# Kernel tuning notes

Measured on AMD Instinct MI355X. Metric: run time of the kernel, lower is better.

## Reference

```python
import jax, jax.numpy as jnp
import numpy as np

N_NODES = 100000
N_EDGES = 1600000
F_IN = 64
F_OUT = 64


def setup_inputs() -> dict:
    key = jax.random.key(0)
    ks = jax.random.split(key, 7)
    x_real = jax.random.normal(ks[0], (N_NODES, F_IN), dtype=jnp.float32)
    x_imag = jax.random.normal(ks[1], (N_NODES, F_IN), dtype=jnp.float32)
    weight = jax.random.normal(ks[2], (2, F_IN, F_OUT), dtype=jnp.float32) * (1.0 / np.sqrt(F_IN))
    bias = jax.random.normal(ks[3], (F_OUT,), dtype=jnp.float32) * 0.01
    norm_real = jax.random.normal(ks[4], (N_EDGES,), dtype=jnp.float32) * 0.1
    norm_imag = jax.random.normal(ks[5], (N_EDGES,), dtype=jnp.float32) * 0.1
    edge_index = jax.random.randint(ks[6], (2, N_EDGES), 0, N_NODES, dtype=jnp.int64 if jax.config.jax_enable_x64 else jnp.int32)
    return {
        "x_real": x_real,
        "x_imag": x_imag,
        "weight": weight,
        "bias": bias,
        "norm_real": norm_real,
        "norm_imag": norm_imag,
        "edge_index": edge_index,
    }


def reference(x_real, x_imag, weight, bias, norm_real, norm_imag, edge_index):
    # SigMaNetConv with i_complex=False: the K=0 term uses i_real=I, i_imag=0,
    # so real_real = x_real @ W0, imag_real = x_imag @ W0, cross terms vanish.
    n = x_real.shape[0]
    src = edge_index[0]  # aggregation target (flow: target_to_source semantics)
    dst = edge_index[1]  # neighbor being gathered (x_j)

    def prop(x, norm):
        # sparse Laplacian matvec: out[src] += norm * x[dst]  -> [N, F]
        return jax.ops.segment_sum(norm[:, None] * x[dst], src, num_segments=n)

    W0, W1 = weight[0], weight[1]
    out_real_real = x_real @ W0 + prop(x_real, norm_real) @ W1
    out_imag_imag = prop(x_imag, norm_imag) @ W1
    out_imag_real = x_imag @ W0 + prop(x_imag, norm_real) @ W1
    out_real_imag = prop(x_real, norm_imag) @ W1

    out_real = out_real_real - out_imag_imag + bias
    out_imag = out_imag_real + out_real_imag + bias
    return out_real, out_imag
```

## Files before the change

kernel.cpp:

```cpp
#include <hip/hip_runtime.h>

#define F 64
typedef unsigned int u32;
typedef unsigned long long u64;
typedef short bf16x8 __attribute__((ext_vector_type(8)));
typedef float f32x4 __attribute__((ext_vector_type(4)));

#define SCAN_BLOCK 1024
#define SCAN_ITEMS 4
#define NPART 8
#define EGRP 16
#define SLICE_MAX 12544
#define SPLITB 512
#define SITEMS 8

__device__ __forceinline__ u32 pack_bf16x2(float lo, float hi) {
    u32 a = __float_as_uint(lo);
    u32 b = __float_as_uint(hi);
    a = (a + 0x7fffu + ((a >> 16) & 1u)) >> 16;
    b = (b + 0x7fffu + ((b >> 16) & 1u)) >> 16;
    return a | (b << 16);
}
__device__ __forceinline__ float unpack_lo(u32 p) { return __uint_as_float(p << 16); }
__device__ __forceinline__ float unpack_hi(u32 p) { return __uint_as_float(p & 0xffff0000u); }

__global__ __launch_bounds__(256) void k_coarse(
    const int* __restrict__ src, int* __restrict__ bcnt,
    const float* __restrict__ weight, unsigned short* __restrict__ Btp,
    int n_edges, int slice, int chunk)
{
    const int t = threadIdx.x;
    if (blockIdx.x == SPLITB) {
        for (int i = t; i < 128 * 64; i += 256) {
            const int f2 = i >> 6;
            const int k  = i & 63;
            const float wv = weight[(f2 >= 64 ? F * F : 0) + k * F + (f2 & 63)];
            Btp[f2 * 64 + (((k >> 3) ^ (f2 & 7)) << 3) + (k & 7)] =
                (unsigned short)(pack_bf16x2(wv, 0.f) & 0xffffu);
        }
        return;
    }
    __shared__ int c[NPART];
    if (t < NPART) c[t] = 0;
    __syncthreads();
    const int cbeg = blockIdx.x * chunk;
    const int cend = min(cbeg + chunk, n_edges);
    for (int e = cbeg + t; e < cend; e += 256)
        atomicAdd(&c[(u32)src[e] / (u32)slice], 1);
    __syncthreads();
    if (t < NPART) bcnt[blockIdx.x * NPART + t] = c[t];
}

__global__ __launch_bounds__(SPLITB) void k_base2(
    const int* __restrict__ bcnt, int* __restrict__ bbase, int* __restrict__ pbase)
{
    __shared__ int wsum[SPLITB / 64];
    __shared__ int total[NPART];
    __shared__ int pb[NPART + 1];
    const int t = threadIdx.x;
    const int lane = t & 63, wid = t >> 6;

    for (int p = 0; p < NPART; ++p) {
        const int v = bcnt[t * NPART + p];
        int incl = v;
#pragma unroll
        for (int d = 1; d < 64; d <<= 1) {
            int x = __shfl_up(incl, d);
            if (lane >= d) incl += x;
        }
        if (lane == 63) wsum[wid] = incl;
        __syncthreads();
        if (wid == 0) {
            int s = (lane < SPLITB / 64) ? wsum[lane] : 0;
#pragma unroll
            for (int d = 1; d < SPLITB / 64; d <<= 1) {
                int x = __shfl_up(s, d);
                if (lane >= d) s += x;
            }
            if (lane < SPLITB / 64) wsum[lane] = s;
        }
        __syncthreads();
        const int excl = (incl - v) + (wid ? wsum[wid - 1] : 0);
        bbase[t * NPART + p] = excl;
        if (t == SPLITB - 1) total[p] = excl + v;
        __syncthreads();
    }
    if (t == 0) {
        int run = 0;
        for (int p = 0; p < NPART; ++p) { pb[p] = run; run += total[p]; }
        pb[NPART] = run;
        for (int p = 0; p <= NPART; ++p) pbase[p] = pb[p];
    }
    __syncthreads();
    for (int p = 0; p < NPART; ++p)
        bbase[t * NPART + p] += pb[p];
}

__global__ __launch_bounds__(256) void k_split(
    const int* __restrict__ ei, const float* __restrict__ nr, const float* __restrict__ ni,
    const int* __restrict__ bbase, u32* __restrict__ ssrc, u64* __restrict__ smrec,
    int n_edges, int slice, int chunk)
{
    __shared__ int cnt[NPART];
    __shared__ int gb[NPART];
    __shared__ int lcur[NPART];
    const int t = threadIdx.x;
    if (t < NPART) lcur[t] = bbase[blockIdx.x * NPART + t];
    const int cbeg = blockIdx.x * chunk;
    const int cend = min(cbeg + chunk, n_edges);

    for (int base = cbeg; base < cend; base += 256 * SITEMS) {
        if (t < NPART) cnt[t] = 0;
        __syncthreads();
        int p[SITEMS], lpos[SITEMS];
        u32 s[SITEMS]; u64 mrec[SITEMS];
#pragma unroll
        for (int j = 0; j < SITEMS; ++j) {
            const int e = base + t + 256 * j;
            if (e < cend) {
                s[j] = (u32)ei[e];
                const u32 d = (u32)ei[n_edges + e];
                const u32 nn = pack_bf16x2(nr[e], ni[e]);
                mrec[j] = (u64)d | ((u64)nn << 32);
                p[j] = (int)(s[j] / (u32)slice);
                lpos[j] = atomicAdd(&cnt[p[j]], 1);
            } else p[j] = -1;
        }
        __syncthreads();
        if (t < NPART) { gb[t] = lcur[t]; lcur[t] += cnt[t]; }
        __syncthreads();
#pragma unroll
        for (int j = 0; j < SITEMS; ++j) {
            if (p[j] >= 0) {
                const int gi = gb[p[j]] + lpos[j];
                ssrc[gi]  = s[j];
                smrec[gi] = mrec[j];
            }
        }
        __syncthreads();
    }
}

__global__ __launch_bounds__(1024) void k_hist8(
    const u32* __restrict__ ssrc, const int* __restrict__ pbase,
    int* __restrict__ priv, int n_nodes, int slice)
{
    __shared__ int h[SLICE_MAX];
    const int p = blockIdx.x & (NPART - 1);
    const int g = blockIdx.x >> 3;
    const int t = threadIdx.x;

    const int lo = p * slice;
    const int hi = min(lo + slice, n_nodes);
    const int sl = hi - lo;
    if (sl <= 0) return;

    for (int i = t; i < sl; i += 1024) h[i] = 0;
    __syncthreads();

    const int pb = pbase[p], pe = pbase[p + 1];
    const long long len = pe - pb;
    const int beg = pb + (int)(len * g / EGRP);
    const int end = pb + (int)(len * (g + 1) / EGRP);
    for (int e = beg + t; e < end; e += 1024)
        atomicAdd(&h[(int)ssrc[e] - lo], 1);
    __syncthreads();

    int* __restrict__ dst = priv + (size_t)g * n_nodes + lo;
    for (int i = t; i < sl; i += 1024) dst[i] = h[i];
}

__global__ __launch_bounds__(1024) void k_scan1(
    const int* __restrict__ priv, int* __restrict__ pre,
    int* __restrict__ partials, int n, int n_nodes)
{
    __shared__ int wsum[16];
    const int t = threadIdx.x;
    const int lane = t & 63, wid = t >> 6;
    const int base = blockIdx.x * (SCAN_BLOCK * SCAN_ITEMS) + t * SCAN_ITEMS;

    int v[SCAN_ITEMS];
    int local = 0;
#pragma unroll
    for (int j = 0; j < SCAN_ITEMS; ++j) {
        const int idx = base + j;
        int c = 0;
        if (idx < n) {
            for (int g = 0; g < EGRP; ++g) c += priv[(size_t)g * n_nodes + idx];
        }
        v[j] = local;
        local += c;
    }
    int incl = local;
#pragma unroll
    for (int d = 1; d < 64; d <<= 1) {
        int x = __shfl_up(incl, d);
        if (lane >= d) incl += x;
    }
    if (lane == 63) wsum[wid] = incl;
    __syncthreads();
    if (wid == 0) {
        int s = (lane < 16) ? wsum[lane] : 0;
#pragma unroll
        for (int d = 1; d < 16; d <<= 1) {
            int x = __shfl_up(s, d);
            if (lane >= d) s += x;
        }
        if (lane < 16) wsum[lane] = s;
    }
    __syncthreads();
    const int texcl = (incl - local) + (wid ? wsum[wid - 1] : 0);
#pragma unroll
    for (int j = 0; j < SCAN_ITEMS; ++j) {
        const int idx = base + j;
        if (idx < n) pre[idx] = texcl + v[j];
    }
    if (t == SCAN_BLOCK - 1) partials[blockIdx.x] = texcl + local;
}

__global__ __launch_bounds__(1024) void k_scan2(
    int* __restrict__ pre, const int* __restrict__ partials,
    int* __restrict__ po, int n, int n_nodes, int n_edges)
{
    __shared__ int s_off;
    const int t = threadIdx.x;
    if (t < 64) {
        int val = (t < blockIdx.x) ? partials[t] : 0;
#pragma unroll
        for (int d = 32; d > 0; d >>= 1) val += __shfl_down(val, d);
        if (t == 0) s_off = val;
    }
    __syncthreads();
    const int boff = s_off;
    const int base = blockIdx.x * (SCAN_BLOCK * SCAN_ITEMS) + t * SCAN_ITEMS;
#pragma unroll
    for (int j = 0; j < SCAN_ITEMS; ++j) {
        const int idx = base + j;
        if (idx < n) {
            const int o = boff + pre[idx];
            pre[idx] = o;
            int running = o;
            for (int g = 0; g < EGRP; ++g) {
                const size_t ix = (size_t)g * n_nodes + idx;
                const int c = po[ix];
                po[ix] = running;
                running += c;
            }
        }
    }
    if (blockIdx.x == 0 && t == 0) pre[n] = n_edges;
}

__global__ __launch_bounds__(1024) void k_place3(
    const u32* __restrict__ ssrc, const u64* __restrict__ smrec,
    const int* __restrict__ pbase, const int* __restrict__ off2,
    u64* __restrict__ meta2, int n_nodes, int slice)
{
    __shared__ int cur[SLICE_MAX];
    const int p = blockIdx.x & (NPART - 1);
    const int g = blockIdx.x >> 3;
    const int t = threadIdx.x;

    const int lo = p * slice;
    const int hi = min(lo + slice, n_nodes);
    const int sl = hi - lo;
    if (sl <= 0) return;

    const int* __restrict__ o2 = off2 + (size_t)g * n_nodes + lo;
    for (int i = t; i < sl; i += 1024) cur[i] = o2[i];
    __syncthreads();

    const int pb = pbase[p], pe = pbase[p + 1];
    const long long len = pe - pb;
    const int beg = pb + (int)(len * g / EGRP);
    const int end = pb + (int)(len * (g + 1) / EGRP);
    for (int e = beg + t; e < end; e += 1024) {
        const int s = (int)ssrc[e];
        const int pos = atomicAdd(&cur[s - lo], 1);
        meta2[pos] = smrec[e];
    }
}

__global__ __launch_bounds__(256, 4) void k_gemm(
    const float* __restrict__ x_real, const float* __restrict__ x_imag,
    const unsigned short* __restrict__ Btp, const float* __restrict__ bias,
    u32* __restrict__ x1p, u32* __restrict__ initp, int n_nodes)
{
    __shared__ unsigned short lds[2 * 128 * 64];
    unsigned short* __restrict__ A  = lds;
    unsigned short* __restrict__ Bt = lds + 128 * 64;

    const int t = threadIdx.x;
    const int base = blockIdx.x * 64;

#pragma unroll
    for (int c = 0; c < 8; ++c) {
        const int fq  = t + 256 * c;
        const int arr = fq >> 10;
        const int rem = fq & 1023;
        const int ln  = rem >> 4;
        const int c4  = rem & 15;
        const int g   = base + ln;
        const float* __restrict__ s = arr ? x_imag : x_real;
        float4 v = make_float4(0.f, 0.f, 0.f, 0.f);
        if (g < n_nodes) v = *(const float4*)(s + (size_t)g * F + c4 * 4);
        const int row  = 2 * ln + arr;
        const int kg   = c4 >> 1;
        const int half = c4 & 1;
        u32* dst = (u32*)&A[row * 64 + ((kg ^ (row & 7)) << 3) + (half << 2)];
        dst[0] = pack_bf16x2(v.x, v.y);
        dst[1] = pack_bf16x2(v.z, v.w);
    }

#pragma unroll
    for (int i = 0; i < 4; ++i) {
        const int idx = t + 256 * i;
        ((uint4*)Bt)[idx] = ((const uint4*)Btp)[idx];
    }
    __syncthreads();

    const int l   = t & 63;
    const int w   = t >> 6;
    const int l15 = l & 15;
    const int lg  = l >> 4;

    f32x4 acc[2][8];
#pragma unroll
    for (int tr = 0; tr < 2; ++tr)
#pragma unroll
        for (int tc = 0; tc < 8; ++tc)
            acc[tr][tc] = (f32x4){0.f, 0.f, 0.f, 0.f};

#pragma unroll
    for (int ks = 0; ks < 2; ++ks) {
        bf16x8 af[2];
#pragma unroll
        for (int tr = 0; tr < 2; ++tr) {
            const int row = w * 32 + tr * 16 + l15;
            const int kg  = ks * 4 + lg;
            af[tr] = *(const bf16x8*)&A[row * 64 + ((kg ^ (row & 7)) << 3)];
        }
#pragma unroll
        for (int tc = 0; tc < 8; ++tc) {
            const int f2 = tc * 16 + l15;
            const int kg = ks * 4 + lg;
            const bf16x8 bfr = *(const bf16x8*)&Bt[f2 * 64 + ((kg ^ (f2 & 7)) << 3)];
#pragma unroll
            for (int tr = 0; tr < 2; ++tr)
                acc[tr][tc] = __builtin_amdgcn_mfma_f32_16x16x32_bf16(
                    af[tr], bfr, acc[tr][tc], 0, 0, 0);
        }
    }

#pragma unroll
    for (int tc = 0; tc < 8; ++tc) {
        const int f2 = tc * 16 + l15;
        const float bv = (f2 < F) ? bias[f2] : 0.f;
#pragma unroll
        for (int tr = 0; tr < 2; ++tr) {
            const int row0 = w * 32 + tr * 16 + lg * 4;
            const int g0 = base + (row0 >> 1);
            const int g1 = g0 + 1;
            const f32x4 a = acc[tr][tc];
            if (f2 < F) {
                if (g0 < n_nodes) initp[(size_t)g0 * F + f2] = pack_bf16x2(a[0] + bv, a[1] + bv);
                if (g1 < n_nodes) initp[(size_t)g1 * F + f2] = pack_bf16x2(a[2] + bv, a[3] + bv);
            } else {
                const int f = f2 - F;
                if (g0 < n_nodes) x1p[(size_t)g0 * F + f] = pack_bf16x2(a[0], a[1]);
                if (g1 < n_nodes) x1p[(size_t)g1 * F + f] = pack_bf16x2(a[2], a[3]);
            }
        }
    }
}

#define APPLY2(m, p, aR, aI)                                  \
    do {                                                      \
        const u32 nnv = (u32)((m) >> 32);                     \
        const float cr = unpack_lo(nnv);                      \
        const float ci = unpack_hi(nnv);                      \
        const float xr = unpack_lo(p);                        \
        const float xi = unpack_hi(p);                        \
        aR = fmaf(cr, xr, fmaf(-ci, xi, aR));                 \
        aI = fmaf(cr, xi, fmaf(ci, xr, aI));                  \
    } while (0)

__global__ __launch_bounds__(256) void k_gather(
    const u32* __restrict__ x1p, const u32* __restrict__ initp,
    const int* __restrict__ offsets, const u64* __restrict__ meta2,
    float* __restrict__ out_real, float* __restrict__ out_imag,
    int n_nodes, int slice)
{
    const int part = blockIdx.x & (NPART - 1);
    const int lane = threadIdx.x & 63;
    const int wip = ((blockIdx.x >> 3) << 2) + (threadIdx.x >> 6);
    const int wpp = (gridDim.x >> 3) << 2;

    const int lo = part * slice;
    const int hi = min(lo + slice, n_nodes);
    if (hi <= lo) return;
    const int chunk = (hi - lo + wpp - 1) / wpp;
    const int nbeg = lo + wip * chunk;
    const int nend = min(nbeg + chunk, hi);

    for (int n = nbeg; n < nend; ++n) {
        const int nu = __builtin_amdgcn_readfirstlane(n);
        const int beg = __builtin_amdgcn_readfirstlane(offsets[nu]);
        const int end = __builtin_amdgcn_readfirstlane(offsets[nu + 1]);

        float aR0 = 0.f, aI0 = 0.f, aR1 = 0.f, aI1 = 0.f;
        float aR2 = 0.f, aI2 = 0.f, aR3 = 0.f, aI3 = 0.f;

        int e = beg;
        for (; e + 8 <= end; e += 8) {
            const u64 m0 = __builtin_nontemporal_load(meta2 + e + 0);
            const u64 m1 = __builtin_nontemporal_load(meta2 + e + 1);
            const u64 m2 = __builtin_nontemporal_load(meta2 + e + 2);
            const u64 m3 = __builtin_nontemporal_load(meta2 + e + 3);
            const u64 m4 = __builtin_nontemporal_load(meta2 + e + 4);
            const u64 m5 = __builtin_nontemporal_load(meta2 + e + 5);
            const u64 m6 = __builtin_nontemporal_load(meta2 + e + 6);
            const u64 m7 = __builtin_nontemporal_load(meta2 + e + 7);
            const u32 p0 = x1p[(size_t)(u32)m0 * F + lane];
            const u32 p1 = x1p[(size_t)(u32)m1 * F + lane];
            const u32 p2 = x1p[(size_t)(u32)m2 * F + lane];
            const u32 p3 = x1p[(size_t)(u32)m3 * F + lane];
            const u32 p4 = x1p[(size_t)(u32)m4 * F + lane];
            const u32 p5 = x1p[(size_t)(u32)m5 * F + lane];
            const u32 p6 = x1p[(size_t)(u32)m6 * F + lane];
            const u32 p7 = x1p[(size_t)(u32)m7 * F + lane];
            APPLY2(m0, p0, aR0, aI0);
            APPLY2(m1, p1, aR1, aI1);
            APPLY2(m2, p2, aR2, aI2);
            APPLY2(m3, p3, aR3, aI3);
            APPLY2(m4, p4, aR0, aI0);
            APPLY2(m5, p5, aR1, aI1);
            APPLY2(m6, p6, aR2, aI2);
            APPLY2(m7, p7, aR3, aI3);
        }
        for (; e + 4 <= end; e += 4) {
            const u64 m0 = __builtin_nontemporal_load(meta2 + e + 0);
            const u64 m1 = __builtin_nontemporal_load(meta2 + e + 1);
            const u64 m2 = __builtin_nontemporal_load(meta2 + e + 2);
            const u64 m3 = __builtin_nontemporal_load(meta2 + e + 3);
            const u32 p0 = x1p[(size_t)(u32)m0 * F + lane];
            const u32 p1 = x1p[(size_t)(u32)m1 * F + lane];
            const u32 p2 = x1p[(size_t)(u32)m2 * F + lane];
            const u32 p3 = x1p[(size_t)(u32)m3 * F + lane];
            APPLY2(m0, p0, aR0, aI0);
            APPLY2(m1, p1, aR1, aI1);
            APPLY2(m2, p2, aR2, aI2);
            APPLY2(m3, p3, aR3, aI3);
        }
        for (; e < end; ++e) {
            const u64 m = __builtin_nontemporal_load(meta2 + e);
            const u32 p = x1p[(size_t)(u32)m * F + lane];
            APPLY2(m, p, aR0, aI0);
        }

        const size_t b = (size_t)nu * F + lane;
        const u32 iw = __builtin_nontemporal_load(initp + b);
        const float oR = unpack_lo(iw) + ((aR0 + aR1) + (aR2 + aR3));
        const float oI = unpack_hi(iw) + ((aI0 + aI1) + (aI2 + aI3));
        __builtin_nontemporal_store(oR, &out_real[b]);
        __builtin_nontemporal_store(oI, &out_imag[b]);
    }
}

__global__ __launch_bounds__(256) void k_init_out(
    const float* __restrict__ x_real, const float* __restrict__ x_imag,
    const float* __restrict__ weight, const float* __restrict__ bias,
    float* __restrict__ out_real, float* __restrict__ out_imag, int n_nodes)
{
    const int lane = threadIdx.x & 63;
    const int waveId = (blockIdx.x * blockDim.x + threadIdx.x) >> 6;
    const int nWaves = (gridDim.x * blockDim.x) >> 6;
    const float* __restrict__ W0 = weight;
    float w0c[F];
#pragma unroll
    for (int k = 0; k < F; ++k) w0c[k] = W0[k * F + lane];
    const float bf = bias[lane];
    for (int n = waveId; n < n_nodes; n += nWaves) {
        const int nu = __builtin_amdgcn_readfirstlane(n);
        const float4* __restrict__ xr4 = (const float4*)(x_real + (size_t)nu * F);
        const float4* __restrict__ xi4 = (const float4*)(x_imag + (size_t)nu * F);
        float gR = 0.f, gI = 0.f;
#pragma unroll
        for (int k4 = 0; k4 < F / 4; ++k4) {
            const float4 vr = xr4[k4];
            const float4 vi = xi4[k4];
            const float xr[4] = {vr.x, vr.y, vr.z, vr.w};
            const float xi[4] = {vi.x, vi.y, vi.z, vi.w};
#pragma unroll
            for (int j = 0; j < 4; ++j) {
                const int k = 4 * k4 + j;
                gR = fmaf(xr[j], w0c[k], gR);
                gI = fmaf(xi[j], w0c[k], gI);
            }
        }
        const size_t b = (size_t)nu * F + lane;
        out_real[b] = gR + bf;
        out_imag[b] = gI + bf;
    }
}

__global__ __launch_bounds__(256) void k_x1_only(
    const float* __restrict__ x_real, const float* __restrict__ x_imag,
    const float* __restrict__ weight, u32* __restrict__ x1p, int n_nodes)
{
    const int lane = threadIdx.x & 63;
    const int waveId = (blockIdx.x * blockDim.x + threadIdx.x) >> 6;
    const int nWaves = (gridDim.x * blockDim.x) >> 6;
    const float* __restrict__ W1 = weight + F * F;
    float w1c[F];
#pragma unroll
    for (int k = 0; k < F; ++k) w1c[k] = W1[k * F + lane];
    for (int n = waveId; n < n_nodes; n += nWaves) {
        const int nu = __builtin_amdgcn_readfirstlane(n);
        const float4* __restrict__ xr4 = (const float4*)(x_real + (size_t)nu * F);
        const float4* __restrict__ xi4 = (const float4*)(x_imag + (size_t)nu * F);
        float aR = 0.f, aI = 0.f;
#pragma unroll
        for (int k4 = 0; k4 < F / 4; ++k4) {
            const float4 vr = xr4[k4];
            const float4 vi = xi4[k4];
            const float xr[4] = {vr.x, vr.y, vr.z, vr.w};
            const float xi[4] = {vi.x, vi.y, vi.z, vi.w};
#pragma unroll
            for (int j = 0; j < 4; ++j) {
                const int k = 4 * k4 + j;
                aR = fmaf(xr[j], w1c[k], aR);
                aI = fmaf(xi[j], w1c[k], aI);
            }
        }
        x1p[(size_t)nu * F + lane] = pack_bf16x2(aR, aI);
    }
}

__global__ __launch_bounds__(256) void k_scatter(
    const u32* __restrict__ x1p, const int* __restrict__ edge_index,
    const float* __restrict__ norm_real, const float* __restrict__ norm_imag,
    float* __restrict__ out_real, float* __restrict__ out_imag, int n_edges)
{
    const long long gid = (long long)blockIdx.x * blockDim.x + threadIdx.x;
    const long long total = (long long)n_edges * 16;
    if (gid >= total) return;
    const int e = (int)(gid >> 4);
    const int c = (int)(gid & 15);
    const int s = edge_index[e];
    const int d = edge_index[n_edges + e];
    const float cr = norm_real[e];
    const float ci = norm_imag[e];
    const uint4 p4 = *(const uint4*)(x1p + (size_t)d * F + c * 4);
    const u32 pp[4] = {p4.x, p4.y, p4.z, p4.w};
    float* __restrict__ pr = out_real + (size_t)s * F + c * 4;
    float* __restrict__ pi = out_imag + (size_t)s * F + c * 4;
#pragma unroll
    for (int j = 0; j < 4; ++j) {
        const float xr = unpack_lo(pp[j]);
        const float xi = unpack_hi(pp[j]);
        unsafeAtomicAdd(pr + j, fmaf(cr, xr, -ci * xi));
        unsafeAtomicAdd(pi + j, fmaf(cr, xi, ci * xr));
    }
}

extern "C" void kernel_launch(void* const* d_in, const int* in_sizes, int n_in,
                              void* d_out, int out_size, void* d_ws, size_t ws_size,
                              hipStream_t stream) {
    const float* x_real     = (const float*)d_in[0];
    const float* x_imag     = (const float*)d_in[1];
    const float* weight     = (const float*)d_in[2];
    const float* bias       = (const float*)d_in[3];
    const float* norm_real  = (const float*)d_in[4];
    const float* norm_imag  = (const float*)d_in[5];
    const int*   edge_index = (const int*)d_in[6];

    const int n_nodes = in_sizes[0] / F;
    const int n_edges = in_sizes[4];
    const int slice   = (n_nodes + NPART - 1) / NPART;

    float* out_real = (float*)d_out;
    float* out_imag = out_real + (size_t)n_nodes * F;
    u32*   initp    = (u32*)d_out;

    char* ws = (char*)d_ws;
    const size_t x1_bytes     = (size_t)n_nodes * F * sizeof(u32);
    const size_t staged_bytes = (size_t)n_edges * 12;
    const size_t A_bytes      = (x1_bytes > staged_bytes ? x1_bytes : staged_bytes + 8);
    const size_t meta_bytes   = (size_t)n_edges * sizeof(u64);
    const size_t off_bytes    = (size_t)(n_nodes + 1) * sizeof(int);
    const size_t priv_bytes   = (size_t)EGRP * n_nodes * sizeof(int);
    const size_t par_bytes    = 64 * sizeof(int);
    const size_t bcnt_bytes   = (size_t)SPLITB * NPART * sizeof(int);
    const size_t bbase_bytes  = (size_t)SPLITB * NPART * sizeof(int);
    const size_t pbase_bytes  = 64 * sizeof(int);
    const size_t btp_bytes    = 128 * 64 * sizeof(unsigned short);
    const size_t need = A_bytes + meta_bytes + off_bytes + priv_bytes + par_bytes
                      + bcnt_bytes + bbase_bytes + pbase_bytes + btp_bytes;

    u32* x1p      = (u32*)ws;
    u32* ssrc     = (u32*)ws;
    u64* smrec    = (u64*)(ws + (size_t)n_edges * sizeof(u32));
    u64* meta2    = (u64*)(ws + A_bytes);
    int* offsets  = (int*)(ws + A_bytes + meta_bytes);
    int* priv     = (int*)(ws + A_bytes + meta_bytes + off_bytes);
    int* partials = (int*)(ws + A_bytes + meta_bytes + off_bytes + priv_bytes);
    int* bcnt     = partials + 64;
    int* bbase    = bcnt + SPLITB * NPART;
    int* pbase    = bbase + SPLITB * NPART;
    unsigned short* Btp = (unsigned short*)(pbase + 64);

    if (ws_size >= need && slice <= SLICE_MAX) {
        const int schunk = (n_edges + SPLITB - 1) / SPLITB;
        k_coarse<<<SPLITB + 1, 256, 0, stream>>>(edge_index, bcnt, weight, Btp,
                                                 n_edges, slice, schunk);
        k_base2<<<1, SPLITB, 0, stream>>>(bcnt, bbase, pbase);
        k_split<<<SPLITB, 256, 0, stream>>>(edge_index, norm_real, norm_imag,
                                            bbase, ssrc, smrec, n_edges, slice, schunk);
        k_hist8<<<NPART * EGRP, 1024, 0, stream>>>(ssrc, pbase, priv, n_nodes, slice);
        const int sblocks = (n_nodes + SCAN_BLOCK * SCAN_ITEMS - 1) / (SCAN_BLOCK * SCAN_ITEMS);
        k_scan1<<<sblocks, SCAN_BLOCK, 0, stream>>>(priv, offsets, partials, n_nodes, n_nodes);
        k_scan2<<<sblocks, SCAN_BLOCK, 0, stream>>>(offsets, partials, priv,
                                                    n_nodes, n_nodes, n_edges);
        k_place3<<<NPART * EGRP, 1024, 0, stream>>>(ssrc, smrec, pbase, priv,
                                                    meta2, n_nodes, slice);
        const int gblocks = (n_nodes + 63) / 64;
        k_gemm<<<gblocks, 256, 0, stream>>>(
            x_real, x_imag, Btp, bias, x1p, initp, n_nodes);
        k_gather<<<2048, 256, 0, stream>>>(
            x1p, initp, offsets, meta2, out_real, out_imag, n_nodes, slice);
    } else {
        k_init_out<<<2048, 256, 0, stream>>>(
            x_real, x_imag, weight, bias, out_real, out_imag, n_nodes);
        k_x1_only<<<2048, 256, 0, stream>>>(x_real, x_imag, weight, x1p, n_nodes);
        const long long work = (long long)n_edges * 16;
        const int blocks = (int)((work + 255) / 256);
        k_scatter<<<blocks, 256, 0, stream>>>(
            x1p, edge_index, norm_real, norm_imag, out_real, out_imag, n_edges);
    }
}
```

Baseline: 191.8 us.

## Fold partition-base scan into consumer kernels and drop k_base2 launch

Removes the single-block k_base2 kernel and has k_split, k_hist8 and k_place3 each recompute the partition bases they need from the per-block bucket counts, using a shared-memory reduction. This removes one serial launch and its global round trip, at the cost of redundant reductions over 4K ints in every block. It also moves the initp load earlier in k_gather so its latency overlaps the edge loop, and doubles the gather grid to 4096 blocks.

```diff
diff --git a/kernel.cpp b/kernel.cpp
--- a/kernel.cpp
+++ b/kernel.cpp
@@ -51,61 +51,47 @@
     if (t < NPART) bcnt[blockIdx.x * NPART + t] = c[t];
 }
 
-__global__ __launch_bounds__(SPLITB) void k_base2(
-    const int* __restrict__ bcnt, int* __restrict__ bbase, int* __restrict__ pbase)
-{
-    __shared__ int wsum[SPLITB / 64];
-    __shared__ int total[NPART];
-    __shared__ int pb[NPART + 1];
-    const int t = threadIdx.x;
-    const int lane = t & 63, wid = t >> 6;
-
-    for (int p = 0; p < NPART; ++p) {
-        const int v = bcnt[t * NPART + p];
-        int incl = v;
-#pragma unroll
-        for (int d = 1; d < 64; d <<= 1) {
-            int x = __shfl_up(incl, d);
-            if (lane >= d) incl += x;
-        }
-        if (lane == 63) wsum[wid] = incl;
-        __syncthreads();
-        if (wid == 0) {
-            int s = (lane < SPLITB / 64) ? wsum[lane] : 0;
-#pragma unroll
-            for (int d = 1; d < SPLITB / 64; d <<= 1) {
-                int x = __shfl_up(s, d);
-                if (lane >= d) s += x;
-            }
-            if (lane < SPLITB / 64) wsum[lane] = s;
-        }
-        __syncthreads();
-        const int excl = (incl - v) + (wid ? wsum[wid - 1] : 0);
-        bbase[t * NPART + p] = excl;
-        if (t == SPLITB - 1) total[p] = excl + v;
-        __syncthreads();
-    }
-    if (t == 0) {
-        int run = 0;
-        for (int p = 0; p < NPART; ++p) { pb[p] = run; run += total[p]; }
-        pb[NPART] = run;
-        for (int p = 0; p <= NPART; ++p) pbase[p] = pb[p];
-    }
-    __syncthreads();
-    for (int p = 0; p < NPART; ++p)
-        bbase[t * NPART + p] += pb[p];
-}
-
 __global__ __launch_bounds__(256) void k_split(
     const int* __restrict__ ei, const float* __restrict__ nr, const float* __restrict__ ni,
-    const int* __restrict__ bbase, u32* __restrict__ ssrc, u64* __restrict__ smrec,
+    const int* __restrict__ bcnt, u32* __restrict__ ssrc, u64* __restrict__ smrec,
     int n_edges, int slice, int chunk)
 {
+    __shared__ int redAll[NPART][32];
+    __shared__ int redPre[NPART][32];
     __shared__ int cnt[NPART];
     __shared__ int gb[NPART];
     __shared__ int lcur[NPART];
     const int t = threadIdx.x;
-    if (t < NPART) lcur[t] = bbase[blockIdx.x * NPART + t];
+
+    {
+        const int p = t & 7, seg = t >> 3;
+        int sAll = 0, sPre = 0;
+        for (int b = seg; b < SPLITB; b += 32) {
+            const int v = bcnt[b * NPART + p];
+            sAll += v;
+            if (b < (int)blockIdx.x) sPre += v;
+        }
+        redAll[p][seg] = sAll;
+        redPre[p][seg] = sPre;
+    }
+    __syncthreads();
+    if (t < NPART) {
+        int a = 0, q = 0;
+#pragma unroll
+        for (int i = 0; i < 32; ++i) { a += redAll[t][i]; q += redPre[t][i]; }
+        redAll[t][0] = a;
+        redPre[t][0] = q;
+    }
+    __syncthreads();
+    if (t == 0) {
+        int run = 0;
+        for (int p = 0; p < NPART; ++p) {
+            lcur[p] = run + redPre[p][0];
+            run += redAll[p][0];
+        }
+    }
+    __syncthreads();
+
     const int cbeg = blockIdx.x * chunk;
     const int cend = min(cbeg + chunk, n_edges);
 
@@ -142,13 +128,37 @@
 }
 
 __global__ __launch_bounds__(1024) void k_hist8(
-    const u32* __restrict__ ssrc, const int* __restrict__ pbase,
+    const u32* __restrict__ ssrc, const int* __restrict__ bcnt,
     int* __restrict__ priv, int n_nodes, int slice)
 {
     __shared__ int h[SLICE_MAX];
+    __shared__ int red[NPART][128];
+    __shared__ int pbs[NPART + 1];
     const int p = blockIdx.x & (NPART - 1);
     const int g = blockIdx.x >> 3;
     const int t = threadIdx.x;
+
+    {
+        const int pp = t & 7, seg = t >> 3;
+        int s = 0;
+#pragma unroll 4
+        for (int b = seg; b < SPLITB; b += 128) s += bcnt[b * NPART + pp];
+        red[pp][seg] = s;
+    }
+    __syncthreads();
+    if (t < NPART) {
+        int a = 0;
+#pragma unroll
+        for (int i = 0; i < 128; ++i) a += red[t][i];
+        red[t][0] = a;
+    }
+    __syncthreads();
+    if (t == 0) {
+        int run = 0;
+        for (int q = 0; q < NPART; ++q) { pbs[q] = run; run += red[q][0]; }
+        pbs[NPART] = run;
+    }
+    __syncthreads();
 
     const int lo = p * slice;
     const int hi = min(lo + slice, n_nodes);
@@ -158,7 +168,7 @@
     for (int i = t; i < sl; i += 1024) h[i] = 0;
     __syncthreads();
 
-    const int pb = pbase[p], pe = pbase[p + 1];
+    const int pb = pbs[p], pe = pbs[p + 1];
     const long long len = pe - pb;
     const int beg = pb + (int)(len * g / EGRP);
     const int end = pb + (int)(len * (g + 1) / EGRP);
@@ -253,13 +263,37 @@
 
 __global__ __launch_bounds__(1024) void k_place3(
     const u32* __restrict__ ssrc, const u64* __restrict__ smrec,
-    const int* __restrict__ pbase, const int* __restrict__ off2,
+    const int* __restrict__ bcnt, const int* __restrict__ off2,
     u64* __restrict__ meta2, int n_nodes, int slice)
 {
     __shared__ int cur[SLICE_MAX];
+    __shared__ int red[NPART][128];
+    __shared__ int pbs[NPART + 1];
     const int p = blockIdx.x & (NPART - 1);
     const int g = blockIdx.x >> 3;
     const int t = threadIdx.x;
+
+    {
+        const int pp = t & 7, seg = t >> 3;
+        int s = 0;
+#pragma unroll 4
+        for (int b = seg; b < SPLITB; b += 128) s += bcnt[b * NPART + pp];
+        red[pp][seg] = s;
+    }
+    __syncthreads();
+    if (t < NPART) {
+        int a = 0;
+#pragma unroll
+        for (int i = 0; i < 128; ++i) a += red[t][i];
+        red[t][0] = a;
+    }
+    __syncthreads();
+    if (t == 0) {
+        int run = 0;
+        for (int q = 0; q < NPART; ++q) { pbs[q] = run; run += red[q][0]; }
+        pbs[NPART] = run;
+    }
+    __syncthreads();
 
     const int lo = p * slice;
     const int hi = min(lo + slice, n_nodes);
@@ -270,7 +304,7 @@
     for (int i = t; i < sl; i += 1024) cur[i] = o2[i];
     __syncthreads();
 
-    const int pb = pbase[p], pe = pbase[p + 1];
+    const int pb = pbs[p], pe = pbs[p + 1];
     const long long len = pe - pb;
     const int beg = pb + (int)(len * g / EGRP);
     const int end = pb + (int)(len * (g + 1) / EGRP);
@@ -407,6 +441,9 @@
         const int nu = __builtin_amdgcn_readfirstlane(n);
         const int beg = __builtin_amdgcn_readfirstlane(offsets[nu]);
         const int end = __builtin_amdgcn_readfirstlane(offsets[nu + 1]);
+
+        const size_t b = (size_t)nu * F + lane;
+        const u32 iw = __builtin_nontemporal_load(initp + b);
 
         float aR0 = 0.f, aI0 = 0.f, aR1 = 0.f, aI1 = 0.f;
         float aR2 = 0.f, aI2 = 0.f, aR3 = 0.f, aI3 = 0.f;
@@ -458,8 +495,6 @@
             APPLY2(m, p, aR0, aI0);
         }
 
-        const size_t b = (size_t)nu * F + lane;
-        const u32 iw = __builtin_nontemporal_load(initp + b);
         const float oR = unpack_lo(iw) + ((aR0 + aR1) + (aR2 + aR3));
         const float oI = unpack_hi(iw) + ((aI0 + aI1) + (aI2 + aI3));
         __builtin_nontemporal_store(oR, &out_real[b]);
@@ -592,11 +627,9 @@
     const size_t priv_bytes   = (size_t)EGRP * n_nodes * sizeof(int);
     const size_t par_bytes    = 64 * sizeof(int);
     const size_t bcnt_bytes   = (size_t)SPLITB * NPART * sizeof(int);
-    const size_t bbase_bytes  = (size_t)SPLITB * NPART * sizeof(int);
-    const size_t pbase_bytes  = 64 * sizeof(int);
     const size_t btp_bytes    = 128 * 64 * sizeof(unsigned short);
     const size_t need = A_bytes + meta_bytes + off_bytes + priv_bytes + par_bytes
-                      + bcnt_bytes + bbase_bytes + pbase_bytes + btp_bytes;
+                      + bcnt_bytes + btp_bytes;
 
     u32* x1p      = (u32*)ws;
     u32* ssrc     = (u32*)ws;
@@ -606,28 +639,25 @@
     int* priv     = (int*)(ws + A_bytes + meta_bytes + off_bytes);
     int* partials = (int*)(ws + A_bytes + meta_bytes + off_bytes + priv_bytes);
     int* bcnt     = partials + 64;
-    int* bbase    = bcnt + SPLITB * NPART;
-    int* pbase    = bbase + SPLITB * NPART;
-    unsigned short* Btp = (unsigned short*)(pbase + 64);
+    unsigned short* Btp = (unsigned short*)(bcnt + SPLITB * NPART);
 
     if (ws_size >= need && slice <= SLICE_MAX) {
         const int schunk = (n_edges + SPLITB - 1) / SPLITB;
         k_coarse<<<SPLITB + 1, 256, 0, stream>>>(edge_index, bcnt, weight, Btp,
                                                  n_edges, slice, schunk);
-        k_base2<<<1, SPLITB, 0, stream>>>(bcnt, bbase, pbase);
         k_split<<<SPLITB, 256, 0, stream>>>(edge_index, norm_real, norm_imag,
-                                            bbase, ssrc, smrec, n_edges, slice, schunk);
-        k_hist8<<<NPART * EGRP, 1024, 0, stream>>>(ssrc, pbase, priv, n_nodes, slice);
+                                            bcnt, ssrc, smrec, n_edges, slice, schunk);
+        k_hist8<<<NPART * EGRP, 1024, 0, stream>>>(ssrc, bcnt, priv, n_nodes, slice);
         const int sblocks = (n_nodes + SCAN_BLOCK * SCAN_ITEMS - 1) / (SCAN_BLOCK * SCAN_ITEMS);
         k_scan1<<<sblocks, SCAN_BLOCK, 0, stream>>>(priv, offsets, partials, n_nodes, n_nodes);
         k_scan2<<<sblocks, SCAN_BLOCK, 0, stream>>>(offsets, partials, priv,
                                                     n_nodes, n_nodes, n_edges);
-        k_place3<<<NPART * EGRP, 1024, 0, stream>>>(ssrc, smrec, pbase, priv,
+        k_place3<<<NPART * EGRP, 1024, 0, stream>>>(ssrc, smrec, bcnt, priv,
                                                     meta2, n_nodes, slice);
         const int gblocks = (n_nodes + 63) / 64;
         k_gemm<<<gblocks, 256, 0, stream>>>(
             x_real, x_imag, Btp, bias, x1p, initp, n_nodes);
-        k_gather<<<2048, 256, 0, stream>>>(
+        k_gather<<<4096, 256, 0, stream>>>(
             x1p, initp, offsets, meta2, out_real, out_imag, n_nodes, slice);
     } else {
         k_init_out<<<2048, 256, 0, stream>>>(
```

New measurement: 187.2 us. -2.4%, faster.
